# Kernel tuning notes

Hardware: AMD Instinct MI355X
Metric: run time of the kernel (lower is better)

The kernel has to match this reference:

```python
import jax, jax.numpy as jnp
import numpy as np

N, M, D, H = 16, 1024, 64, 4  # batch, num_node, dim_in==dim_hid, num_head
NEG_SLOPE = 0.2


def setup_inputs() -> dict:
    key = jax.random.key(0)
    ks = jax.random.split(key, 10)
    s = 1.0 / np.sqrt(D)
    inp = {
        "x": jax.random.normal(ks[0], (N, M, D), dtype=jnp.float32),
        "edge": jnp.zeros((N, M, M), dtype=jnp.float32),  # unused by the module
        # stacked per-head Linear(dim_in, dim_hid) params: weight (H, D_out, D_in), bias (H, D_out)
        "Wk": (jax.random.normal(ks[1], (H, D, D), dtype=jnp.float32) * s),
        "bk": (jax.random.normal(ks[2], (H, D), dtype=jnp.float32) * s),
        "Wq": (jax.random.normal(ks[3], (H, D, D), dtype=jnp.float32) * s),
        "bq": (jax.random.normal(ks[4], (H, D), dtype=jnp.float32) * s),
        "Wv": (jax.random.normal(ks[5], (H, D, D), dtype=jnp.float32) * s),
        "bv": (jax.random.normal(ks[6], (H, D), dtype=jnp.float32) * s),
        # decoder: Linear(dim_hid*num_head -> dim_in)
        "Wdec": (jax.random.normal(ks[7], (D, H * D), dtype=jnp.float32) / np.sqrt(H * D)),
        "bdec": (jax.random.normal(ks[8], (D,), dtype=jnp.float32) / np.sqrt(H * D)),
    }
    return inp


def reference(x, edge, Wk, bk, Wq, bq, Wv, bv, Wdec, bdec):
    # x: (N, M, D). Per head h: K = x @ Wk[h].T + bk[h], etc.
    K = jnp.einsum("nmd,hed->nhme", x, Wk) + bk[None, :, None, :]  # (N,H,M,D)
    Q = jnp.einsum("nmd,hed->nhme", x, Wq) + bq[None, :, None, :]
    V = jnp.einsum("nmd,hed->nhme", x, Wv) + bv[None, :, None, :]
    # alpha[n,h,i,j] = K[n,h,i] . Q[n,h,j]  (sender=K row i, receiver=Q row j)
    alpha = jnp.einsum("nhie,nhje->nhij", K, Q)  # (N,H,M,M)
    alpha = jax.nn.leaky_relu(alpha, NEG_SLOPE)
    alpha = jax.nn.softmax(alpha, axis=-1)
    agg = jnp.einsum("nhij,nhje->nhie", alpha, V)  # (N,H,M,D)
    dx = jax.nn.leaky_relu(agg, NEG_SLOPE) - x[:, None, :, :]  # (N,H,M,D)
    # concat heads along feature dim (head 0 first): (N, M, H*D)
    dx = dx.transpose(0, 2, 1, 3).reshape(N, M, H * D)
    return dx @ Wdec.T + bdec  # (N, M, D)
```

## Files before the change

### kernel.cpp

```cpp
#include <hip/hip_runtime.h>
#include <hip/hip_bf16.h>


#define NB 16
#define MM 1024
#define DD 64
#define HH 4
#define NEG 0.2f
#define AST 72
#define DST 264
#define LOG2E 1.44269504088896f

typedef __attribute__((ext_vector_type(8))) short bf16x8;
typedef __attribute__((ext_vector_type(8))) _Float16 f16x8;
typedef __attribute__((ext_vector_type(16))) float f32x16;
typedef __attribute__((ext_vector_type(4))) unsigned int uint4v;
typedef __attribute__((ext_vector_type(2))) unsigned int uint2v;

__device__ inline unsigned short f2bf(float f) {
  unsigned int u = __builtin_bit_cast(unsigned int, f);
  unsigned int r = (u + 0x7FFFu + ((u >> 16) & 1u)) >> 16;
  return (unsigned short)r;
}
__device__ inline unsigned short f2h(float f) {
  _Float16 h = (_Float16)f;
  return __builtin_bit_cast(unsigned short, h);
}
__device__ inline unsigned int pk_bf16(float lo, float hi) {
  unsigned int r;
  asm("v_cvt_pk_bf16_f32 %0, %1, %2" : "=v"(r) : "v"(lo), "v"(hi));
  return r;
}
__device__ inline void swap32(unsigned int& a, unsigned int& b) {
  uint2v r = __builtin_amdgcn_permlane32_swap(a, b, false, false);
  a = r.x;
  b = r.y;
}

__global__ __launch_bounds__(256) void prep_kernel(
    const float* __restrict__ Wk, const float* __restrict__ Wq,
    const float* __restrict__ Wv, const float* __restrict__ Wdec,
    unsigned short* __restrict__ Wf) {
  const int idx = (blockIdx.x * 256 + threadIdx.x) * 4;
  const int seg = idx >> 14, local = idx & 16383;
  const float* src = seg == 0 ? Wk : seg == 1 ? Wq : seg == 2 ? Wv : Wdec;
  float4 v = *(const float4*)&src[local];
  unsigned short p[4] = {f2h(v.x), f2h(v.y), f2h(v.z), f2h(v.w)};
  *(uint2*)&Wf[idx] = *(uint2*)p;
}

__global__ __launch_bounds__(256) void proj_kernel(
    const float* __restrict__ x, const unsigned short* __restrict__ Wf,
    const float* __restrict__ bk, const float* __restrict__ bq, const float* __restrict__ bv,
    unsigned short* __restrict__ Kf, unsigned short* __restrict__ Qf,
    unsigned short* __restrict__ Vtg) {
  __shared__ unsigned short xs[64 * AST];
  __shared__ unsigned short ob[64 * AST];
  const int t = threadIdx.x;
  const int r0 = blockIdx.x * 64;
  const int combo = blockIdx.y, mat = combo >> 2, h = combo & 3;
  const int n = r0 >> 10, ml = r0 & 1023;
  const float* bias = mat == 0 ? bk : (mat == 1 ? bq : bv);

#pragma unroll
  for (int rep = 0; rep < 2; ++rep) {
    int idx = rep * 256 + t, row = idx >> 3, c8 = (idx & 7) * 8;
    float4 a = *(const float4*)&x[(size_t)(r0 + row) * DD + c8];
    float4 b = *(const float4*)&x[(size_t)(r0 + row) * DD + c8 + 4];
    unsigned short p[8] = {f2h(a.x), f2h(a.y), f2h(a.z), f2h(a.w),
                           f2h(b.x), f2h(b.y), f2h(b.z), f2h(b.w)};
    *(uint4*)&xs[row * AST + c8] = *(uint4*)p;
  }
  __syncthreads();

  const int w = t >> 6, lane = t & 63, m31 = lane & 31, hf = lane >> 5;
  const int mi = w >> 1, ne = w & 1;
  const int ecol = h * 64 + ne * 32 + m31;
  const float bb = bias[ecol];

  f32x16 C;
#pragma unroll
  for (int r = 0; r < 16; ++r) C[r] = 0.f;
#pragma unroll
  for (int ks = 0; ks < 4; ++ks) {
    f16x8 xa = *(f16x8*)&xs[(mi * 32 + m31) * AST + ks * 16 + hf * 8];
    f16x8 wb = *(const f16x8*)&Wf[(size_t)mat * 16384 + (size_t)ecol * DD + ks * 16 + hf * 8];
    C = __builtin_amdgcn_mfma_f32_32x32x16_f16(xa, wb, C, 0, 0, 0);
  }

  if (mat < 2) {
    const float ksc = (mat == 0) ? LOG2E : 1.0f;
#pragma unroll
    for (int r = 0; r < 16; ++r) {
      int rr = (r & 3) + 8 * (r >> 2) + 4 * hf;
      ob[(mi * 32 + rr) * AST + ne * 32 + m31] = f2h((C[r] + bb) * ksc);
    }
  } else {
#pragma unroll
    for (int r = 0; r < 16; ++r) {
      int rr = (r & 3) + 8 * (r >> 2) + 4 * hf;
      ob[(ne * 32 + m31) * AST + mi * 32 + rr] = f2bf(C[r] + bb);
    }
  }
  __syncthreads();

  if (mat == 0) {
    const size_t obase = (((size_t)n * HH + h) * MM + ml) * DD;
#pragma unroll
    for (int rep = 0; rep < 2; ++rep) {
      int idx = rep * 256 + t, row = idx >> 3, c8 = (idx & 7) * 8;
      *(uint4*)&Kf[obase + (size_t)row * DD + c8] = *(uint4*)&ob[row * AST + c8];
    }
  } else if (mat == 1) {
    const size_t obase = (((size_t)n * HH + h) * MM + ml) * DD;
#pragma unroll
    for (int rep = 0; rep < 2; ++rep) {
      int idx = rep * 256 + t;
      int jb32l = idx >> 8, ks = (idx >> 6) & 3, hf2 = (idx >> 5) & 1, mr = idx & 31;
      *(uint4*)&Qf[obase + (size_t)idx * 8] =
          *(uint4*)&ob[(jb32l * 32 + mr) * AST + ks * 16 + hf2 * 8];
    }
  } else {
    const size_t obaseT = (((size_t)n * HH + h) * DD) * MM + (size_t)(ml >> 6) * 4096;
#pragma unroll
    for (int rep = 0; rep < 2; ++rep) {
      int idx = rep * 256 + t;
      int ks = idx >> 7, eh = (idx >> 6) & 1, hf2 = (idx >> 5) & 1, mr = idx & 31;
      *(uint4*)&Vtg[obaseT + (size_t)idx * 8] =
          *(uint4*)&ob[(eh * 32 + mr) * AST + ks * 16 + hf2 * 8];
    }
  }
}


#define LOADF(qa0_, qa1_, bv0_, bv1_, jtn)                         \
  do {                                                             \
    const unsigned short* Qj_ = Qp + (size_t)(jtn) * 4096;         \
    const unsigned short* Vj_ = Vp + (size_t)(jtn) * 4096;         \
    _Pragma("unroll") for (int ks = 0; ks < 4; ++ks) {             \
      qa0_[ks] = *(const f16x8*)&Qj_[ks * 512 + loff];             \
      qa1_[ks] = *(const f16x8*)&Qj_[2048 + ks * 512 + loff];      \
      bv0_[ks] = *(const bf16x8*)&Vj_[ks * 1024 + loff];           \
      bv1_[ks] = *(const bf16x8*)&Vj_[ks * 1024 + 512 + loff];     \
    }                                                              \
  } while (0)

#define SOFTPACK(C_, dst0_, dst1_)                                             \
  do {                                                                         \
    _Pragma("unroll") for (int r = 0; r < 16; ++r) {                           \
      float s = C_[r];                                                         \
      s = fmaxf(s, NEG * s);                                                   \
      s = __builtin_amdgcn_exp2f(s);                                           \
      lac += s;                                                                \
      C_[r] = s;                                                               \
    }                                                                          \
    {                                                                          \
      unsigned int p01 = pk_bf16(C_[0], C_[1]), p23 = pk_bf16(C_[2], C_[3]);   \
      unsigned int p45 = pk_bf16(C_[4], C_[5]), p67 = pk_bf16(C_[6], C_[7]);   \
      swap32(p01, p45);                                                        \
      swap32(p23, p67);                                                        \
      uint4v wlo = {p01, p23, p45, p67};                                       \
      dst0_ = __builtin_bit_cast(bf16x8, wlo);                                 \
      unsigned int p89 = pk_bf16(C_[8], C_[9]), pAB = pk_bf16(C_[10], C_[11]); \
      unsigned int pCD = pk_bf16(C_[12], C_[13]), pEF = pk_bf16(C_[14], C_[15]); \
      swap32(p89, pCD);                                                        \
      swap32(pAB, pEF);                                                        \
      uint4v whi = {p89, pAB, pCD, pEF};                                       \
      dst1_ = __builtin_bit_cast(bf16x8, whi);                                 \
    }                                                                          \
  } while (0)

#define COMPUTE(qa0_, qa1_, bv0_, bv1_)                                         \
  do {                                                                          \
    bf16x8 pa[4];                                                               \
    f32x16 C;                                                                   \
    _Pragma("unroll") for (int r = 0; r < 16; ++r) C[r] = 0.f;                  \
    _Pragma("unroll") for (int ks = 0; ks < 4; ++ks)                            \
        C = __builtin_amdgcn_mfma_f32_32x32x16_f16(qa0_[ks], kfrag[ks], C, 0, 0, 0); \
    SOFTPACK(C, pa[0], pa[1]);                                                  \
    _Pragma("unroll") for (int r = 0; r < 16; ++r) C[r] = 0.f;                  \
    _Pragma("unroll") for (int ks = 0; ks < 4; ++ks)                            \
        C = __builtin_amdgcn_mfma_f32_32x32x16_f16(qa1_[ks], kfrag[ks], C, 0, 0, 0); \
    SOFTPACK(C, pa[2], pa[3]);                                                  \
    _Pragma("unroll") for (int ks = 0; ks < 4; ++ks) {                          \
      agg0 = __builtin_amdgcn_mfma_f32_32x32x16_bf16(pa[ks], bv0_[ks], agg0, 0, 0, 0); \
      agg1 = __builtin_amdgcn_mfma_f32_32x32x16_bf16(pa[ks], bv1_[ks], agg1, 0, 0, 0); \
    }                                                                           \
  } while (0)

__global__ __launch_bounds__(256, 2) void attn_kernel(
    const unsigned short* __restrict__ Kf, const unsigned short* __restrict__ Qf,
    const unsigned short* __restrict__ Vtg, const float* __restrict__ x,
    unsigned short* __restrict__ DX) {
  __shared__ __align__(16) unsigned short sm[128 * AST];

  const int t = threadIdx.x;
  const int w = t >> 6, lane = t & 63;
  const int m31 = lane & 31, hf = lane >> 5;

  const int slot = blockIdx.x + 8 * (blockIdx.y + HH * (int)blockIdx.z);
  const int xcd = slot & 7, within = slot >> 3;
  const int grp = xcd * 8 + (within >> 3);
  const int ib = within & 7;
  const int n = grp >> 2, h = grp & 3;
  const int i0 = ib * 128;

  const size_t base = (((size_t)n * HH + h) * MM) * DD;
  const size_t baseT = (((size_t)n * HH + h) * DD) * MM;
  const unsigned short* Qp = Qf + base;
  const unsigned short* Vp = Vtg + baseT;

  f16x8 kfrag[4];
#pragma unroll
  for (int ks = 0; ks < 4; ++ks)
    kfrag[ks] = *(const f16x8*)&Kf[base + (size_t)(i0 + w * 32 + m31) * DD + ks * 16 + hf * 8];

  f32x16 agg0, agg1;
#pragma unroll
  for (int r = 0; r < 16; ++r) { agg0[r] = 0.f; agg1[r] = 0.f; }
  float lac = 0.f;

  const int loff = hf * 256 + m31 * 8;

  f16x8 Aq0[4], Aq1[4], Bq0[4], Bq1[4];
  bf16x8 Av0[4], Av1[4], Bv0[4], Bv1[4];

  LOADF(Aq0, Aq1, Av0, Av1, 0);
  for (int g = 0; g < 8; ++g) {
    LOADF(Bq0, Bq1, Bv0, Bv1, 2 * g + 1);
    COMPUTE(Aq0, Aq1, Av0, Av1);
    if (g < 7) LOADF(Aq0, Aq1, Av0, Av1, 2 * g + 2);
    COMPUTE(Bq0, Bq1, Bv0, Bv1);
  }

  const float lsum = lac + __shfl_xor(lac, 32);

#pragma unroll
  for (int r = 0; r < 16; ++r) {
    const int rr = (r & 3) + 8 * (r >> 2) + 4 * hf;
    const float rl = 1.0f / __shfl(lsum, rr);
    const size_t xrow = ((size_t)n * MM + i0 + w * 32 + rr) * DD;
    float v0 = agg0[r] * rl;
    v0 = fmaxf(v0, NEG * v0);
    v0 -= x[xrow + m31];
    sm[(w * 32 + rr) * AST + m31] = f2h(v0);
    float v1 = agg1[r] * rl;
    v1 = fmaxf(v1, NEG * v1);
    v1 -= x[xrow + 32 + m31];
    sm[(w * 32 + rr) * AST + 32 + m31] = f2h(v1);
  }
  __syncthreads();
#pragma unroll
  for (int rep = 0; rep < 4; ++rep) {
    const int idx = rep * 256 + t, row = idx >> 3, cc = (idx & 7) * 8;
    *(uint4*)&DX[((size_t)n * MM + i0 + row) * (HH * DD) + h * DD + cc] =
        *(uint4*)&sm[row * AST + cc];
  }
}

__global__ __launch_bounds__(256) void dec_kernel(
    const unsigned short* __restrict__ DX, const unsigned short* __restrict__ Wdf,
    const float* __restrict__ bdec, float* __restrict__ out) {
  __shared__ unsigned short dxs[64 * DST];
  const int t = threadIdx.x;
  const int w = t >> 6, lane = t & 63, m31 = lane & 31, hf = lane >> 5;
  const int mi = w >> 1, nd = w & 1;
  const int r0 = blockIdx.x * 64;
#pragma unroll
  for (int rep = 0; rep < 8; ++rep) {
    int idx = rep * 256 + t, row = idx >> 5, c8 = (idx & 31) * 8;
    *(uint4*)&dxs[row * DST + c8] = *(const uint4*)&DX[(size_t)(r0 + row) * 256 + c8];
  }
  __syncthreads();
  const float bb = bdec[nd * 32 + m31];
  f32x16 C;
#pragma unroll
  for (int r = 0; r < 16; ++r) C[r] = 0.f;
#pragma unroll
  for (int ks = 0; ks < 16; ++ks) {
    f16x8 aD = *(f16x8*)&dxs[(mi * 32 + m31) * DST + ks * 16 + hf * 8];
    f16x8 bW = *(const f16x8*)&Wdf[(size_t)(nd * 32 + m31) * 256 + ks * 16 + hf * 8];
    C = __builtin_amdgcn_mfma_f32_32x32x16_f16(aD, bW, C, 0, 0, 0);
  }
#pragma unroll
  for (int r = 0; r < 16; ++r) {
    int rr = (r & 3) + 8 * (r >> 2) + 4 * hf;
    out[(size_t)(r0 + mi * 32 + rr) * DD + nd * 32 + m31] = C[r] + bb;
  }
}

extern "C" void kernel_launch(void* const* d_in, const int* in_sizes, int n_in,
                              void* d_out, int out_size, void* d_ws, size_t ws_size,
                              hipStream_t stream) {
  const float* x    = (const float*)d_in[0];
  const float* Wk   = (const float*)d_in[2];
  const float* bk   = (const float*)d_in[3];
  const float* Wq   = (const float*)d_in[4];
  const float* bq   = (const float*)d_in[5];
  const float* Wv   = (const float*)d_in[6];
  const float* bv   = (const float*)d_in[7];
  const float* Wdec = (const float*)d_in[8];
  const float* bdec = (const float*)d_in[9];
  float* out = (float*)d_out;

  const size_t seg = (size_t)NB * HH * MM * DD;
  unsigned short* Kf  = (unsigned short*)d_ws;
  unsigned short* Qf  = Kf + seg;
  unsigned short* Vt  = Qf + seg;
  unsigned short* DXp = Vt + seg;
  unsigned short* Wf  = DXp + seg;
  unsigned short* Wdf = Wf + 3 * 16384;

  prep_kernel<<<64, 256, 0, stream>>>(Wk, Wq, Wv, Wdec, Wf);
  proj_kernel<<<dim3(256, 12), 256, 0, stream>>>(x, Wf, bk, bq, bv, Kf, Qf, Vt);
  attn_kernel<<<dim3(8, HH, NB), 256, 0, stream>>>(Kf, Qf, Vt, x, DXp);
  dec_kernel<<<NB * MM / 64, 256, 0, stream>>>(DXp, Wdf, bdec, out);
}
```

Before: 151.1 us.

## Fuse decoder projection into attention kernel with per-block head reduction

Removes the separate decoder kernel and the DX intermediate round-trip through global memory. Each 512-thread block now covers 64 rows of one batch for all four heads, with one head per wave pair. Each wave multiplies its head's dx slice by the matching Wdec columns and accumulates into a shared fp32 tile via LDS atomics. The bias is added during the final store. This trades one kernel launch and the global DX traffic for LDS atomic contention and a changed grid and block shape.

New measurement: 162.2 us. 7.4% more time.

```diff
diff --git a/kernel.cpp b/kernel.cpp
--- a/kernel.cpp
+++ b/kernel.cpp
@@ -8,7 +8,7 @@
 #define HH 4
 #define NEG 0.2f
 #define AST 72
-#define DST 264
+#define OST 65
 #define LOG2E 1.44269504088896f
 
 typedef __attribute__((ext_vector_type(8))) short bf16x8;
@@ -188,22 +188,26 @@
     }                                                                           \
   } while (0)
 
-__global__ __launch_bounds__(256, 2) void attn_kernel(
+__global__ __launch_bounds__(512, 2) void attn_kernel(
     const unsigned short* __restrict__ Kf, const unsigned short* __restrict__ Qf,
     const unsigned short* __restrict__ Vtg, const float* __restrict__ x,
-    unsigned short* __restrict__ DX) {
-  __shared__ __align__(16) unsigned short sm[128 * AST];
+    const unsigned short* __restrict__ Wdf, const float* __restrict__ bdec,
+    float* __restrict__ out) {
+  __shared__ __align__(16) unsigned short dxs[8 * 32 * AST];
+  __shared__ float outacc[64 * OST];
 
   const int t = threadIdx.x;
   const int w = t >> 6, lane = t & 63;
   const int m31 = lane & 31, hf = lane >> 5;
-
-  const int slot = blockIdx.x + 8 * (blockIdx.y + HH * (int)blockIdx.z);
-  const int xcd = slot & 7, within = slot >> 3;
-  const int grp = xcd * 8 + (within >> 3);
-  const int ib = within & 7;
-  const int n = grp >> 2, h = grp & 3;
-  const int i0 = ib * 128;
+  const int istrip = w >> 2, h = w & 3;
+
+  const int slot = blockIdx.x + 16 * (int)blockIdx.y;
+  const int val = (slot & 7) * 32 + (slot >> 3);
+  const int n = val >> 4, ib = val & 15;
+  const int i0 = ib * 64;
+
+  for (int idx = t; idx < 64 * OST; idx += 512) outacc[idx] = 0.f;
+  __syncthreads();
 
   const size_t base = (((size_t)n * HH + h) * MM) * DD;
   const size_t baseT = (((size_t)n * HH + h) * DD) * MM;
@@ -213,7 +217,8 @@
   f16x8 kfrag[4];
 #pragma unroll
   for (int ks = 0; ks < 4; ++ks)
-    kfrag[ks] = *(const f16x8*)&Kf[base + (size_t)(i0 + w * 32 + m31) * DD + ks * 16 + hf * 8];
+    kfrag[ks] =
+        *(const f16x8*)&Kf[base + (size_t)(i0 + istrip * 32 + m31) * DD + ks * 16 + hf * 8];
 
   f32x16 agg0, agg1;
 #pragma unroll
@@ -235,57 +240,52 @@
 
   const float lsum = lac + __shfl_xor(lac, 32);
 
+  unsigned short* dxw = dxs + w * (32 * AST);
 #pragma unroll
   for (int r = 0; r < 16; ++r) {
     const int rr = (r & 3) + 8 * (r >> 2) + 4 * hf;
     const float rl = 1.0f / __shfl(lsum, rr);
-    const size_t xrow = ((size_t)n * MM + i0 + w * 32 + rr) * DD;
+    const size_t xrow = ((size_t)n * MM + i0 + istrip * 32 + rr) * DD;
     float v0 = agg0[r] * rl;
     v0 = fmaxf(v0, NEG * v0);
     v0 -= x[xrow + m31];
-    sm[(w * 32 + rr) * AST + m31] = f2h(v0);
+    dxw[rr * AST + m31] = f2h(v0);
     float v1 = agg1[r] * rl;
     v1 = fmaxf(v1, NEG * v1);
     v1 -= x[xrow + 32 + m31];
-    sm[(w * 32 + rr) * AST + 32 + m31] = f2h(v1);
+    dxw[rr * AST + 32 + m31] = f2h(v1);
+  }
+
+  f32x16 Co0, Co1;
+#pragma unroll
+  for (int r = 0; r < 16; ++r) { Co0[r] = 0.f; Co1[r] = 0.f; }
+#pragma unroll
+  for (int ks = 0; ks < 4; ++ks) {
+    f16x8 aD = *(f16x8*)&dxw[m31 * AST + ks * 16 + hf * 8];
+    f16x8 w0 = *(const f16x8*)&Wdf[(size_t)m31 * 256 + h * 64 + ks * 16 + hf * 8];
+    f16x8 w1 = *(const f16x8*)&Wdf[(size_t)(32 + m31) * 256 + h * 64 + ks * 16 + hf * 8];
+    Co0 = __builtin_amdgcn_mfma_f32_32x32x16_f16(aD, w0, Co0, 0, 0, 0);
+    Co1 = __builtin_amdgcn_mfma_f32_32x32x16_f16(aD, w1, Co1, 0, 0, 0);
+  }
+
+#pragma unroll
+  for (int r = 0; r < 16; ++r) {
+    const int rr = (r & 3) + 8 * (r >> 2) + 4 * hf;
+    atomicAdd(&outacc[(istrip * 32 + rr) * OST + m31], Co0[r]);
+    atomicAdd(&outacc[(istrip * 32 + rr) * OST + 32 + m31], Co1[r]);
   }
   __syncthreads();
-#pragma unroll
-  for (int rep = 0; rep < 4; ++rep) {
-    const int idx = rep * 256 + t, row = idx >> 3, cc = (idx & 7) * 8;
-    *(uint4*)&DX[((size_t)n * MM + i0 + row) * (HH * DD) + h * DD + cc] =
-        *(uint4*)&sm[row * AST + cc];
-  }
-}
-
-__global__ __launch_bounds__(256) void dec_kernel(
-    const unsigned short* __restrict__ DX, const unsigned short* __restrict__ Wdf,
-    const float* __restrict__ bdec, float* __restrict__ out) {
-  __shared__ unsigned short dxs[64 * DST];
-  const int t = threadIdx.x;
-  const int w = t >> 6, lane = t & 63, m31 = lane & 31, hf = lane >> 5;
-  const int mi = w >> 1, nd = w & 1;
-  const int r0 = blockIdx.x * 64;
-#pragma unroll
-  for (int rep = 0; rep < 8; ++rep) {
-    int idx = rep * 256 + t, row = idx >> 5, c8 = (idx & 31) * 8;
-    *(uint4*)&dxs[row * DST + c8] = *(const uint4*)&DX[(size_t)(r0 + row) * 256 + c8];
-  }
-  __syncthreads();
-  const float bb = bdec[nd * 32 + m31];
-  f32x16 C;
-#pragma unroll
-  for (int r = 0; r < 16; ++r) C[r] = 0.f;
-#pragma unroll
-  for (int ks = 0; ks < 16; ++ks) {
-    f16x8 aD = *(f16x8*)&dxs[(mi * 32 + m31) * DST + ks * 16 + hf * 8];
-    f16x8 bW = *(const f16x8*)&Wdf[(size_t)(nd * 32 + m31) * 256 + ks * 16 + hf * 8];
-    C = __builtin_amdgcn_mfma_f32_32x32x16_f16(aD, bW, C, 0, 0, 0);
-  }
-#pragma unroll
-  for (int r = 0; r < 16; ++r) {
-    int rr = (r & 3) + 8 * (r >> 2) + 4 * hf;
-    out[(size_t)(r0 + mi * 32 + rr) * DD + nd * 32 + m31] = C[r] + bb;
+
+#pragma unroll
+  for (int rep = 0; rep < 2; ++rep) {
+    const int idx = rep * 512 + t;
+    const int row = idx >> 4, c4 = (idx & 15) * 4;
+    float4 v;
+    v.x = outacc[row * OST + c4 + 0] + bdec[c4 + 0];
+    v.y = outacc[row * OST + c4 + 1] + bdec[c4 + 1];
+    v.z = outacc[row * OST + c4 + 2] + bdec[c4 + 2];
+    v.w = outacc[row * OST + c4 + 3] + bdec[c4 + 3];
+    *(float4*)&out[((size_t)n * MM + i0 + row) * DD + c4] = v;
   }
 }
 
@@ -313,6 +313,5 @@
 
   prep_kernel<<<64, 256, 0, stream>>>(Wk, Wq, Wv, Wdec, Wf);
   proj_kernel<<<dim3(256, 12), 256, 0, stream>>>(x, Wf, bk, bq, bv, Kf, Qf, Vt);
-  attn_kernel<<<dim3(8, HH, NB), 256, 0, stream>>>(Kf, Qf, Vt, x, DXp);
-  dec_kernel<<<NB * MM / 64, 256, 0, stream>>>(DXp, Wdf, bdec, out);
-}
+  attn_kernel<<<dim3(16, 16), 512, 0, stream>>>(Kf, Qf, Vt, x, Wdf, bdec, out);
+}
```
